# Kernel tuning notes

Measured on AMD Instinct MI355X. Metric: run time of the kernel, lower is better.

## Reference

```python
import jax, jax.numpy as jnp
import numpy as np

B, T, F, H = 256, 1024, 64, 128
DT = 1.0
EPS = 1e-5


def _layer_norm(h, g, b):
    mu = jnp.mean(h, axis=-1, keepdims=True)
    var = jnp.var(h, axis=-1, keepdims=True)
    return (h - mu) * jax.lax.rsqrt(var + EPS) * g + b


def setup_inputs() -> dict:
    key = jax.random.key(0)
    ks = jax.random.split(key, 8)
    def xavier(k, shape):
        fan_in, fan_out = shape[1], shape[0]
        lim = np.sqrt(6.0 / (fan_in + fan_out))
        return jax.random.uniform(k, shape, jnp.float32, -lim, lim)
    return {
        "x": jax.random.normal(ks[0], (B, T, F), jnp.float32),
        # layer 0 (input_dim=F)
        "Wh0": xavier(ks[1], (H, H)), "bh0": jnp.zeros((H,), jnp.float32),
        "Wx0": xavier(ks[2], (H, F)), "bx0": jnp.zeros((H,), jnp.float32),
        "Wt0": xavier(ks[3], (H, F)), "bt0": jnp.zeros((H,), jnp.float32),
        "tau0": jnp.ones((H,), jnp.float32),
        "g0": jnp.ones((H,), jnp.float32), "be0": jnp.zeros((H,), jnp.float32),
        # layer 1 (input_dim=H)
        "Wh1": xavier(ks[4], (H, H)), "bh1": jnp.zeros((H,), jnp.float32),
        "Wx1": xavier(ks[5], (H, H)), "bx1": jnp.zeros((H,), jnp.float32),
        "Wt1": xavier(ks[6], (H, H)), "bt1": jnp.zeros((H,), jnp.float32),
        "tau1": jnp.ones((H,), jnp.float32),
        "g1": jnp.ones((H,), jnp.float32), "be1": jnp.zeros((H,), jnp.float32),
    }


def _cell(x_t, h, Wh, bh, Wx, bx, Wt, bt, tau_base):
    f = jnp.tanh(h @ Wh.T + bh + x_t @ Wx.T + bx)        # (B,H)
    tau = tau_base + jax.nn.softplus(x_t @ Wt.T + bt)     # (B,H)
    return h + (DT / tau) * (-h + f)


def reference(x, Wh0, bh0, Wx0, bx0, Wt0, bt0, tau0, g0, be0,
              Wh1, bh1, Wx1, bx1, Wt1, bt1, tau1, g1, be1):
    xT = jnp.transpose(x, (1, 0, 2))  # (T,B,F)

    def step(carry, x_t):
        h0, h1 = carry
        h0 = _layer_norm(_cell(x_t, h0, Wh0, bh0, Wx0, bx0, Wt0, bt0, tau0), g0, be0)
        h1 = _layer_norm(_cell(h0, h1, Wh1, bh1, Wx1, bx1, Wt1, bt1, tau1), g1, be1)
        return (h0, h1), None

    h_init = (jnp.zeros((x.shape[0], H), x.dtype), jnp.zeros((x.shape[0], H), x.dtype))
    (h0, h1), _ = jax.lax.scan(step, h_init, xT)
    return h1  # hidden_dim == latent_dim, no proj
```

## Files before the change

kernel.cpp:

```cpp
#include <hip/hip_runtime.h>
#include <stdint.h>


#define B_ 256
#define T_ 1024
#define F_ 64
#define H_ 128
#define EPS_ 1e-5f
#define NT_ 512

typedef _Float16 h2 __attribute__((ext_vector_type(2)));
typedef _Float16 h8 __attribute__((ext_vector_type(8)));
typedef float f32x4 __attribute__((ext_vector_type(4)));
typedef __fp16  f16v2 __attribute__((ext_vector_type(2)));

__device__ __forceinline__ h2 pkf16(float a, float b) {
  union { f16v2 f; h2 h; } c;
  c.f = __builtin_amdgcn_cvt_pkrtz(a, b);
  return c.h;
}
__device__ __forceinline__ uint32_t as_u32(h2 h) { union { h2 h; uint32_t u; } c; c.h = h; return c.u; }

__device__ __forceinline__ void wg_barrier() {
  asm volatile("s_waitcnt lgkmcnt(0)\n\ts_barrier" ::: "memory");
}

#if __has_builtin(__builtin_amdgcn_rsqf)
__device__ __forceinline__ float rsq_fast(float x) { return __builtin_amdgcn_rsqf(x); }
#else
__device__ __forceinline__ float rsq_fast(float x) { return rsqrtf(x); }
#endif

#if __has_builtin(__builtin_amdgcn_update_dpp)
template <int CTRL>
__device__ __forceinline__ float dpp_add(float v) {
  union { float f; int i; } a, b;
  a.f = v;
  b.i = __builtin_amdgcn_update_dpp(0, a.i, CTRL, 0xf, 0xf, true);
  return v + b.f;
}
__device__ __forceinline__ float red16(float v) {
  v = dpp_add<0x128>(v);
  v = dpp_add<0x124>(v);
  v = dpp_add<0x122>(v);
  v = dpp_add<0x121>(v);
  return v;
}
#else
__device__ __forceinline__ float red16(float v) {
  v += __shfl_xor(v, 1); v += __shfl_xor(v, 2);
  v += __shfl_xor(v, 4); v += __shfl_xor(v, 8);
  return v;
}
#endif

__device__ __forceinline__ h8 packfrag(const float* p) {
  float4 a = *(const float4*)p;
  float4 b = *(const float4*)(p + 4);
  union { h2 h[4]; h8 v; } c;
  c.h[0] = pkf16(a.x, a.y); c.h[1] = pkf16(a.z, a.w);
  c.h[2] = pkf16(b.x, b.y); c.h[3] = pkf16(b.z, b.w);
  return c.v;
}
__device__ __forceinline__ h8 packfrag_g(const float* w, const float* gv, const float* bv,
                                         float& dg, float& dbe) {
  float4 a = *(const float4*)w;
  float4 b = *(const float4*)(w + 4);
  float4 ga = *(const float4*)gv;
  float4 gb = *(const float4*)(gv + 4);
  float4 ba = *(const float4*)bv;
  float4 bb = *(const float4*)(bv + 4);
  float w0 = a.x*ga.x, w1 = a.y*ga.y, w2 = a.z*ga.z, w3 = a.w*ga.w;
  float w4 = b.x*gb.x, w5 = b.y*gb.y, w6 = b.z*gb.z, w7 = b.w*gb.w;
  dg  += (w0 + w1) + (w2 + w3) + (w4 + w5) + (w6 + w7);
  dbe += a.x*ba.x + a.y*ba.y + a.z*ba.z + a.w*ba.w
       + b.x*bb.x + b.y*bb.y + b.z*bb.z + b.w*bb.w;
  union { h2 h[4]; h8 v; } c;
  c.h[0] = pkf16(w0, w1); c.h[1] = pkf16(w2, w3);
  c.h[2] = pkf16(w4, w5); c.h[3] = pkf16(w6, w7);
  return c.v;
}
__device__ __forceinline__ h8 ldfrag(const uint32_t* p) {
  union { uint4 u; h8 v; } c;
  c.u = *(const uint4*)p;
  return c.v;
}

__device__ __forceinline__ float tanh_fast(float a) {
  float aa = fabsf(a);
  float e  = __expf(2.f * aa);
  float th = 1.f - 2.f * __builtin_amdgcn_rcpf(e + 1.f);
  return copysignf(th, a);
}
__device__ __forceinline__ float softplus_fast(float x) {
  return (x > 20.f) ? x : __logf(1.f + __expf(x));
}

#define MFMA16(A_, B_, C_) __builtin_amdgcn_mfma_f32_16x16x32_f16(A_, B_, C_, 0, 0, 0)

__global__ void __attribute__((amdgpu_flat_work_group_size(NT_, NT_)))
                __attribute__((amdgpu_waves_per_eu(2, 2)))
ltc_scan(
    const float* __restrict__ x,
    const float* __restrict__ Wh0, const float* __restrict__ bh0,
    const float* __restrict__ Wx0, const float* __restrict__ bx0,
    const float* __restrict__ Wt0, const float* __restrict__ bt0,
    const float* __restrict__ tau0, const float* __restrict__ g0,
    const float* __restrict__ be0,
    const float* __restrict__ Wh1, const float* __restrict__ bh1,
    const float* __restrict__ Wx1, const float* __restrict__ bx1,
    const float* __restrict__ Wt1, const float* __restrict__ bt1,
    const float* __restrict__ tau1, const float* __restrict__ g1,
    const float* __restrict__ be1,
    float* __restrict__ out)
{
  __shared__ __align__(16) uint32_t h0p[2][64];
  __shared__ __align__(16) uint32_t h1p[2][64];
  __shared__ __align__(16) uint32_t x4[4][32];
  __shared__ __align__(16) float    part[4][4];

  const int tid = threadIdx.x;
  const int wid = tid >> 6;
  const int l   = tid & 63;
  const int g4  = (l >> 4) << 2;
  const int g8  = (l >> 4) << 3;
  const int b   = blockIdx.x;
  const float* xg = x + (size_t)b * (T_ * F_);
  const bool selT1 = (l & 16) != 0;

  if (tid < 128) { ((uint32_t*)h0p)[tid] = 0u; ((uint32_t*)h1p)[tid] = 0u; }
  if (tid < 16)  ((float*)part)[tid] = 0.f;
  if (tid < 32) {
    float2 a = *(const float2*)(xg + 2 * tid);
    float2 c = *(const float2*)(xg + F_ + 2 * tid);
    x4[0][tid] = as_u32(pkf16(a.x, a.y));
    x4[1][tid] = as_u32(pkf16(c.x, c.y));
  }
  __syncthreads();

  if (wid < 4) {
    const int c0 = wid * 32 + (l & 15);
    const int ct = wid * 32 + (l & 31);
    h8 wh0[4], wh1[4], wx0[2], wx1[2], wt0[2], wt1[2];
    float cg, cb;
    {
      float dg0 = 0.f, db0 = 0.f, dg1 = 0.f, db1 = 0.f;
      const float* p0 = Wh0 + c0 * H_ + g8;
      const float* p1 = Wh0 + (c0 + 16) * H_ + g8;
      #pragma unroll
      for (int m = 0; m < 4; ++m) {
        wh0[m] = packfrag_g(p0 + 32 * m, g0 + g8 + 32 * m, be0 + g8 + 32 * m, dg0, db0);
        wh1[m] = packfrag_g(p1 + 32 * m, g0 + g8 + 32 * m, be0 + g8 + 32 * m, dg1, db1);
      }
      dg0 += __shfl_xor(dg0, 16); dg0 += __shfl_xor(dg0, 32);
      db0 += __shfl_xor(db0, 16); db0 += __shfl_xor(db0, 32);
      dg1 += __shfl_xor(dg1, 16); dg1 += __shfl_xor(dg1, 32);
      db1 += __shfl_xor(db1, 16); db1 += __shfl_xor(db1, 32);
      cg = selT1 ? dg1 : dg0; cb = selT1 ? db1 : db0;
      const float* q0 = Wx0 + c0 * F_ + g8;
      const float* q1 = Wx0 + (c0 + 16) * F_ + g8;
      const float* r0 = Wt0 + c0 * F_ + g8;
      const float* r1 = Wt0 + (c0 + 16) * F_ + g8;
      #pragma unroll
      for (int m = 0; m < 2; ++m) {
        wx0[m] = packfrag(q0 + 32 * m); wx1[m] = packfrag(q1 + 32 * m);
        wt0[m] = packfrag(r0 + 32 * m); wt1[m] = packfrag(r1 + 32 * m);
      }
    }
    const float bhx = bh0[ct] + bx0[ct];
    const float btr = bt0[ct], taub = tau0[ct], gr = g0[ct], ber = be0[ct];
    const int  widx = wid * 16 + ((l & 31) >> 1);
    const bool wlane = ((l & 33) == 0);
    const bool st = (wid == 0) && (l < 32);

    float hcp = 0.f;
    float2 xc0, xc1;
    if (st) {
      xc0 = *(const float2*)(xg + 2 * F_ + 2 * l);
      xc1 = *(const float2*)(xg + 3 * F_ + 2 * l);
    }

    #pragma unroll 4
    for (int i = 0; i <= T_; ++i) {
      const float2 stt = *(const float2*)&part[(i + 3) & 3][0];
      if (st) {
        x4[(i + 2) & 3][l] = as_u32(pkf16(xc0.x, xc0.y));
        xc0 = xc1;
        int tn = (i + 4 < T_) ? (i + 4) : (T_ - 1);
        xc1 = *(const float2*)(xg + tn * F_ + 2 * l);
      }
      const uint32_t* ub = h0p[(i + 1) & 1];
      const uint32_t* xb = x4[i & 3];
      f32x4 aH0 = {0.f,0.f,0.f,0.f}, aH1 = {0.f,0.f,0.f,0.f};
      f32x4 aX0 = {0.f,0.f,0.f,0.f}, aX1 = {0.f,0.f,0.f,0.f};
      f32x4 aT0 = {0.f,0.f,0.f,0.f}, aT1 = {0.f,0.f,0.f,0.f};
      #pragma unroll
      for (int m = 0; m < 4; ++m) {
        h8 af = ldfrag(ub + m * 16 + g4);
        aH0 = MFMA16(af, wh0[m], aH0);
        aH1 = MFMA16(af, wh1[m], aH1);
      }
      #pragma unroll
      for (int m = 0; m < 2; ++m) {
        h8 xf = ldfrag(xb + m * 16 + g4);
        aX0 = MFMA16(xf, wx0[m], aX0);
        aX1 = MFMA16(xf, wx1[m], aX1);
        aT0 = MFMA16(xf, wt0[m], aT0);
        aT1 = MFMA16(xf, wt1[m], aT1);
      }
      float aH = selT1 ? aH1[0] : aH0[0];
      float aX = selT1 ? aX1[0] : aX0[0];
      float aT = selT1 ? aT1[0] : aT0[0];
      float mu = stt.x * (1.f / 128.f);
      float m2 = stt.y * (1.f / 128.f);
      float rstd = rsq_fast(m2 - mu * mu + EPS_);
      float fl = (i > 0) ? 1.f : 0.f;
      float sc = fl * rstd;
      float pa = fmaf(sc, aH, fmaf(-sc * mu, cg, fl * cb)) + aX + bhx;
      float pt = aT + btr;
      float f   = tanh_fast(pa);
      float tau = taub + softplus_fast(pt);
      float hold = fl * fmaf((hcp - mu) * rstd, gr, ber);
      float hc  = fmaf(f - hold, __builtin_amdgcn_rcpf(tau), hold);
      float hc2 = __shfl_xor(hc, 1);
      if (wlane) h0p[i & 1][widx] = as_u32(pkf16(hc, hc2));
      float v = (l & 32) ? hc * hc : hc;
      v = red16(v); v += __shfl_xor(v, 16);
      if (l == 0)  atomicAdd(&part[i & 3][0], v);
      if (l == 32) atomicAdd(&part[i & 3][1], v);
      hcp = hc;
      wg_barrier();
    }
  } else {
    const int c0 = (wid - 4) * 32 + (l & 15);
    const int ct = (wid - 4) * 32 + (l & 31);
    h8 vh0[4], vh1[4], vx0[4], vx1[4], vt0[4], vt1[4];
    float cAg, cAb, cBg, cBb, cTg, cTb;
    {
      float d1=0.f,d2=0.f,d3=0.f,d4=0.f,d5=0.f,d6=0.f;
      float e1=0.f,e2=0.f,e3=0.f,e4=0.f,e5=0.f,e6=0.f;
      const float* p0 = Wh1 + c0 * H_ + g8;
      const float* p1 = Wh1 + (c0 + 16) * H_ + g8;
      const float* q0 = Wx1 + c0 * H_ + g8;
      const float* q1 = Wx1 + (c0 + 16) * H_ + g8;
      const float* r0 = Wt1 + c0 * H_ + g8;
      const float* r1 = Wt1 + (c0 + 16) * H_ + g8;
      #pragma unroll
      for (int m = 0; m < 4; ++m) {
        vh0[m] = packfrag_g(p0 + 32 * m, g1 + g8 + 32 * m, be1 + g8 + 32 * m, d1, d2);
        vh1[m] = packfrag_g(p1 + 32 * m, g1 + g8 + 32 * m, be1 + g8 + 32 * m, e1, e2);
        vx0[m] = packfrag_g(q0 + 32 * m, g0 + g8 + 32 * m, be0 + g8 + 32 * m, d3, d4);
        vx1[m] = packfrag_g(q1 + 32 * m, g0 + g8 + 32 * m, be0 + g8 + 32 * m, e3, e4);
        vt0[m] = packfrag_g(r0 + 32 * m, g0 + g8 + 32 * m, be0 + g8 + 32 * m, d5, d6);
        vt1[m] = packfrag_g(r1 + 32 * m, g0 + g8 + 32 * m, be0 + g8 + 32 * m, e5, e6);
      }
      d1 += __shfl_xor(d1, 16); d1 += __shfl_xor(d1, 32);
      d2 += __shfl_xor(d2, 16); d2 += __shfl_xor(d2, 32);
      d3 += __shfl_xor(d3, 16); d3 += __shfl_xor(d3, 32);
      d4 += __shfl_xor(d4, 16); d4 += __shfl_xor(d4, 32);
      d5 += __shfl_xor(d5, 16); d5 += __shfl_xor(d5, 32);
      d6 += __shfl_xor(d6, 16); d6 += __shfl_xor(d6, 32);
      e1 += __shfl_xor(e1, 16); e1 += __shfl_xor(e1, 32);
      e2 += __shfl_xor(e2, 16); e2 += __shfl_xor(e2, 32);
      e3 += __shfl_xor(e3, 16); e3 += __shfl_xor(e3, 32);
      e4 += __shfl_xor(e4, 16); e4 += __shfl_xor(e4, 32);
      e5 += __shfl_xor(e5, 16); e5 += __shfl_xor(e5, 32);
      e6 += __shfl_xor(e6, 16); e6 += __shfl_xor(e6, 32);
      cAg = selT1 ? e1 : d1; cAb = selT1 ? e2 : d2;
      cBg = selT1 ? e3 : d3; cBb = selT1 ? e4 : d4;
      cTg = selT1 ? e5 : d5; cTb = selT1 ? e6 : d6;
    }
    const float bhx = bh1[ct] + bx1[ct];
    const float btr = bt1[ct], taub = tau1[ct], gr = g1[ct], ber = be1[ct];
    const int  widx = (wid - 4) * 16 + ((l & 31) >> 1);
    const bool wlane = ((l & 33) == 0);
    const bool zt = (tid == NT_ - 1);

    float hcp = 0.f;
    #pragma unroll 2
    for (int i = 0; i <= T_; ++i) {
      const float4 P = *(const float4*)&part[(i + 3) & 3][0];
      if (zt) *(float4*)&part[(i + 2) & 3][0] = make_float4(0.f, 0.f, 0.f, 0.f);
      const uint32_t* u1b = h1p[(i + 1) & 1];
      const uint32_t* u0b = h0p[(i + 1) & 1];
      f32x4 aA0 = {0.f,0.f,0.f,0.f}, aA1 = {0.f,0.f,0.f,0.f};
      f32x4 aB0 = {0.f,0.f,0.f,0.f}, aB1 = {0.f,0.f,0.f,0.f};
      f32x4 aT0 = {0.f,0.f,0.f,0.f}, aT1 = {0.f,0.f,0.f,0.f};
      #pragma unroll
      for (int m = 0; m < 4; ++m) {
        h8 af = ldfrag(u1b + m * 16 + g4);
        aA0 = MFMA16(af, vh0[m], aA0);
        aA1 = MFMA16(af, vh1[m], aA1);
      }
      #pragma unroll
      for (int m = 0; m < 4; ++m) {
        h8 f0 = ldfrag(u0b + m * 16 + g4);
        aB0 = MFMA16(f0, vx0[m], aB0);
        aB1 = MFMA16(f0, vx1[m], aB1);
        aT0 = MFMA16(f0, vt0[m], aT0);
        aT1 = MFMA16(f0, vt1[m], aT1);
      }
      float aA = selT1 ? aA1[0] : aA0[0];
      float aB = selT1 ? aB1[0] : aB0[0];
      float aT = selT1 ? aT1[0] : aT0[0];
      float mu0 = P.x * (1.f / 128.f), m20 = P.y * (1.f / 128.f);
      float mu1 = P.z * (1.f / 128.f), m21 = P.w * (1.f / 128.f);
      float rstd0 = rsq_fast(m20 - mu0 * mu0 + EPS_);
      float rstd1 = rsq_fast(m21 - mu1 * mu1 + EPS_);
      float fl0 = (i > 0) ? 1.f : 0.f;
      float fl1 = (i > 1) ? 1.f : 0.f;
      float sc0 = fl0 * rstd0, sc1 = fl1 * rstd1;
      float pa = fmaf(sc1, aA, fmaf(-sc1 * mu1, cAg, fl1 * cAb))
               + fmaf(sc0, aB, fmaf(-sc0 * mu0, cBg, fl0 * cBb)) + bhx;
      float pt = fmaf(sc0, aT, fmaf(-sc0 * mu0, cTg, fl0 * cTb)) + btr;
      float f   = tanh_fast(pa);
      float tau = taub + softplus_fast(pt);
      float hold = fl1 * fmaf((hcp - mu1) * rstd1, gr, ber);
      float hc  = fmaf(f - hold, __builtin_amdgcn_rcpf(tau), hold);
      float hc2 = __shfl_xor(hc, 1);
      bool we = (i > 0);
      if (we && wlane) h1p[i & 1][widx] = as_u32(pkf16(hc, hc2));
      float v = (l & 32) ? hc * hc : hc;
      v = red16(v); v += __shfl_xor(v, 16);
      if (we && l == 0)  atomicAdd(&part[i & 3][2], v);
      if (we && l == 32) atomicAdd(&part[i & 3][3], v);
      if (we) hcp = hc;
      wg_barrier();
    }
    {
      float mu1 = part[T_ & 3][2] * (1.f / 128.f);
      float m21 = part[T_ & 3][3] * (1.f / 128.f);
      float rstd1 = rsq_fast(m21 - mu1 * mu1 + EPS_);
      float hn = fmaf((hcp - mu1) * rstd1, gr, ber);
      if (l < 32) out[b * H_ + ct] = hn;
    }
  }
}

extern "C" void kernel_launch(void* const* d_in, const int* in_sizes, int n_in,
                              void* d_out, int out_size, void* d_ws, size_t ws_size,
                              hipStream_t stream) {
  const float* x    = (const float*)d_in[0];
  const float* Wh0  = (const float*)d_in[1];
  const float* bh0  = (const float*)d_in[2];
  const float* Wx0  = (const float*)d_in[3];
  const float* bx0  = (const float*)d_in[4];
  const float* Wt0  = (const float*)d_in[5];
  const float* bt0  = (const float*)d_in[6];
  const float* tau0 = (const float*)d_in[7];
  const float* g0   = (const float*)d_in[8];
  const float* be0  = (const float*)d_in[9];
  const float* Wh1  = (const float*)d_in[10];
  const float* bh1  = (const float*)d_in[11];
  const float* Wx1  = (const float*)d_in[12];
  const float* bx1  = (const float*)d_in[13];
  const float* Wt1  = (const float*)d_in[14];
  const float* bt1  = (const float*)d_in[15];
  const float* tau1 = (const float*)d_in[16];
  const float* g1   = (const float*)d_in[17];
  const float* be1  = (const float*)d_in[18];
  float* out        = (float*)d_out;

  ltc_scan<<<B_, NT_, 0, stream>>>(x, Wh0, bh0, Wx0, bx0, Wt0, bt0, tau0, g0, be0,
                                   Wh1, bh1, Wx1, bx1, Wt1, bt1, tau1, g1, be1, out);
}
```

Baseline: 1.009 ms.

## Pass normalized layer-0 state to layer 1 and replace LDS atomics with per-wave partials

Layer-0 waves now write the already layer-normed previous state (hold) into a 4-deep ring buffer, so layer-1 waves can run its input matmul on normalized values and no longer need gamma/beta folding for the Wx/Wt terms or layer-0 statistics. LayerNorm sums are written as per-wave float2 partials and summed by readers, which removes the LDS atomicAdds and the slot-zeroing store. Layer 1 is pipelined one extra step behind, so the loop runs T+2 iterations. The cost is extra LDS traffic, an additional shuffle and store per layer-0 step, and one more barrier iteration.

```diff
diff --git a/kernel.cpp b/kernel.cpp
--- a/kernel.cpp
+++ b/kernel.cpp
@@ -116,8 +116,10 @@
 {
   __shared__ __align__(16) uint32_t h0p[2][64];
   __shared__ __align__(16) uint32_t h1p[2][64];
+  __shared__ __align__(16) uint32_t hn0p[4][64];
   __shared__ __align__(16) uint32_t x4[4][32];
-  __shared__ __align__(16) float    part[4][4];
+  __shared__ __align__(16) float2   p0s[4][4];
+  __shared__ __align__(16) float2   p1s[4][4];
 
   const int tid = threadIdx.x;
   const int wid = tid >> 6;
@@ -129,7 +131,7 @@
   const bool selT1 = (l & 16) != 0;
 
   if (tid < 128) { ((uint32_t*)h0p)[tid] = 0u; ((uint32_t*)h1p)[tid] = 0u; }
-  if (tid < 16)  ((float*)part)[tid] = 0.f;
+  if (tid < 32)  { ((float*)p0s)[tid] = 0.f; ((float*)p1s)[tid] = 0.f; }
   if (tid < 32) {
     float2 a = *(const float2*)(xg + 2 * tid);
     float2 c = *(const float2*)(xg + F_ + 2 * tid);
@@ -181,64 +183,71 @@
     }
 
     #pragma unroll 4
-    for (int i = 0; i <= T_; ++i) {
-      const float2 stt = *(const float2*)&part[(i + 3) & 3][0];
-      if (st) {
-        x4[(i + 2) & 3][l] = as_u32(pkf16(xc0.x, xc0.y));
-        xc0 = xc1;
-        int tn = (i + 4 < T_) ? (i + 4) : (T_ - 1);
-        xc1 = *(const float2*)(xg + tn * F_ + 2 * l);
-      }
-      const uint32_t* ub = h0p[(i + 1) & 1];
-      const uint32_t* xb = x4[i & 3];
-      f32x4 aH0 = {0.f,0.f,0.f,0.f}, aH1 = {0.f,0.f,0.f,0.f};
-      f32x4 aX0 = {0.f,0.f,0.f,0.f}, aX1 = {0.f,0.f,0.f,0.f};
-      f32x4 aT0 = {0.f,0.f,0.f,0.f}, aT1 = {0.f,0.f,0.f,0.f};
-      #pragma unroll
-      for (int m = 0; m < 4; ++m) {
-        h8 af = ldfrag(ub + m * 16 + g4);
-        aH0 = MFMA16(af, wh0[m], aH0);
-        aH1 = MFMA16(af, wh1[m], aH1);
-      }
-      #pragma unroll
-      for (int m = 0; m < 2; ++m) {
-        h8 xf = ldfrag(xb + m * 16 + g4);
-        aX0 = MFMA16(xf, wx0[m], aX0);
-        aX1 = MFMA16(xf, wx1[m], aX1);
-        aT0 = MFMA16(xf, wt0[m], aT0);
-        aT1 = MFMA16(xf, wt1[m], aT1);
-      }
-      float aH = selT1 ? aH1[0] : aH0[0];
-      float aX = selT1 ? aX1[0] : aX0[0];
-      float aT = selT1 ? aT1[0] : aT0[0];
-      float mu = stt.x * (1.f / 128.f);
-      float m2 = stt.y * (1.f / 128.f);
-      float rstd = rsq_fast(m2 - mu * mu + EPS_);
-      float fl = (i > 0) ? 1.f : 0.f;
-      float sc = fl * rstd;
-      float pa = fmaf(sc, aH, fmaf(-sc * mu, cg, fl * cb)) + aX + bhx;
-      float pt = aT + btr;
-      float f   = tanh_fast(pa);
-      float tau = taub + softplus_fast(pt);
-      float hold = fl * fmaf((hcp - mu) * rstd, gr, ber);
-      float hc  = fmaf(f - hold, __builtin_amdgcn_rcpf(tau), hold);
-      float hc2 = __shfl_xor(hc, 1);
-      if (wlane) h0p[i & 1][widx] = as_u32(pkf16(hc, hc2));
-      float v = (l & 32) ? hc * hc : hc;
-      v = red16(v); v += __shfl_xor(v, 16);
-      if (l == 0)  atomicAdd(&part[i & 3][0], v);
-      if (l == 32) atomicAdd(&part[i & 3][1], v);
-      hcp = hc;
+    for (int p = 0; p <= T_ + 1; ++p) {
+      if (p <= T_) {
+        const int i = p;
+        const float4* sp = (const float4*)&p0s[(i + 3) & 3][0];
+        float4 sa = sp[0], sb = sp[1];
+        float ss  = (sa.x + sa.z) + (sb.x + sb.z);
+        float s2s = (sa.y + sa.w) + (sb.y + sb.w);
+        if (st) {
+          x4[(i + 2) & 3][l] = as_u32(pkf16(xc0.x, xc0.y));
+          xc0 = xc1;
+          int tn = (i + 4 < T_) ? (i + 4) : (T_ - 1);
+          xc1 = *(const float2*)(xg + tn * F_ + 2 * l);
+        }
+        const uint32_t* ub = h0p[(i + 1) & 1];
+        const uint32_t* xb = x4[i & 3];
+        f32x4 aH0 = {0.f,0.f,0.f,0.f}, aH1 = {0.f,0.f,0.f,0.f};
+        f32x4 aX0 = {0.f,0.f,0.f,0.f}, aX1 = {0.f,0.f,0.f,0.f};
+        f32x4 aT0 = {0.f,0.f,0.f,0.f}, aT1 = {0.f,0.f,0.f,0.f};
+        #pragma unroll
+        for (int m = 0; m < 4; ++m) {
+          h8 af = ldfrag(ub + m * 16 + g4);
+          aH0 = MFMA16(af, wh0[m], aH0);
+          aH1 = MFMA16(af, wh1[m], aH1);
+        }
+        #pragma unroll
+        for (int m = 0; m < 2; ++m) {
+          h8 xf = ldfrag(xb + m * 16 + g4);
+          aX0 = MFMA16(xf, wx0[m], aX0);
+          aX1 = MFMA16(xf, wx1[m], aX1);
+          aT0 = MFMA16(xf, wt0[m], aT0);
+          aT1 = MFMA16(xf, wt1[m], aT1);
+        }
+        float aH = selT1 ? aH1[0] : aH0[0];
+        float aX = selT1 ? aX1[0] : aX0[0];
+        float aT = selT1 ? aT1[0] : aT0[0];
+        float mu = ss * (1.f / 128.f);
+        float m2 = s2s * (1.f / 128.f);
+        float rstd = rsq_fast(m2 - mu * mu + EPS_);
+        float fl = (i > 0) ? 1.f : 0.f;
+        float sc = fl * rstd;
+        float pa = fmaf(sc, aH, fmaf(-sc * mu, cg, fl * cb)) + aX + bhx;
+        float pt = aT + btr;
+        float f   = tanh_fast(pa);
+        float tau = taub + softplus_fast(pt);
+        float hold = fl * fmaf((hcp - mu) * rstd, gr, ber);
+        float hc  = fmaf(f - hold, __builtin_amdgcn_rcpf(tau), hold);
+        float hn2 = __shfl_xor(hold, 1);
+        if (wlane) hn0p[(i + 3) & 3][widx] = as_u32(pkf16(hold, hn2));
+        float hc2 = __shfl_xor(hc, 1);
+        if (wlane) h0p[i & 1][widx] = as_u32(pkf16(hc, hc2));
+        float v = (l & 32) ? hc * hc : hc;
+        v = red16(v); v += __shfl_xor(v, 16);
+        float v2 = __shfl_down(v, 32);
+        if (l == 0) p0s[i & 3][wid] = make_float2(v, v2);
+        hcp = hc;
+      }
       wg_barrier();
     }
   } else {
     const int c0 = (wid - 4) * 32 + (l & 15);
     const int ct = (wid - 4) * 32 + (l & 31);
     h8 vh0[4], vh1[4], vx0[4], vx1[4], vt0[4], vt1[4];
-    float cAg, cAb, cBg, cBb, cTg, cTb;
+    float cAg, cAb;
     {
-      float d1=0.f,d2=0.f,d3=0.f,d4=0.f,d5=0.f,d6=0.f;
-      float e1=0.f,e2=0.f,e3=0.f,e4=0.f,e5=0.f,e6=0.f;
+      float d1 = 0.f, d2 = 0.f, e1 = 0.f, e2 = 0.f;
       const float* p0 = Wh1 + c0 * H_ + g8;
       const float* p1 = Wh1 + (c0 + 16) * H_ + g8;
       const float* q0 = Wx1 + c0 * H_ + g8;
@@ -249,87 +258,80 @@
       for (int m = 0; m < 4; ++m) {
         vh0[m] = packfrag_g(p0 + 32 * m, g1 + g8 + 32 * m, be1 + g8 + 32 * m, d1, d2);
         vh1[m] = packfrag_g(p1 + 32 * m, g1 + g8 + 32 * m, be1 + g8 + 32 * m, e1, e2);
-        vx0[m] = packfrag_g(q0 + 32 * m, g0 + g8 + 32 * m, be0 + g8 + 32 * m, d3, d4);
-        vx1[m] = packfrag_g(q1 + 32 * m, g0 + g8 + 32 * m, be0 + g8 + 32 * m, e3, e4);
-        vt0[m] = packfrag_g(r0 + 32 * m, g0 + g8 + 32 * m, be0 + g8 + 32 * m, d5, d6);
-        vt1[m] = packfrag_g(r1 + 32 * m, g0 + g8 + 32 * m, be0 + g8 + 32 * m, e5, e6);
+        vx0[m] = packfrag(q0 + 32 * m); vx1[m] = packfrag(q1 + 32 * m);
+        vt0[m] = packfrag(r0 + 32 * m); vt1[m] = packfrag(r1 + 32 * m);
       }
       d1 += __shfl_xor(d1, 16); d1 += __shfl_xor(d1, 32);
       d2 += __shfl_xor(d2, 16); d2 += __shfl_xor(d2, 32);
-      d3 += __shfl_xor(d3, 16); d3 += __shfl_xor(d3, 32);
-      d4 += __shfl_xor(d4, 16); d4 += __shfl_xor(d4, 32);
-      d5 += __shfl_xor(d5, 16); d5 += __shfl_xor(d5, 32);
-      d6 += __shfl_xor(d6, 16); d6 += __shfl_xor(d6, 32);
       e1 += __shfl_xor(e1, 16); e1 += __shfl_xor(e1, 32);
       e2 += __shfl_xor(e2, 16); e2 += __shfl_xor(e2, 32);
-      e3 += __shfl_xor(e3, 16); e3 += __shfl_xor(e3, 32);
-      e4 += __shfl_xor(e4, 16); e4 += __shfl_xor(e4, 32);
-      e5 += __shfl_xor(e5, 16); e5 += __shfl_xor(e5, 32);
-      e6 += __shfl_xor(e6, 16); e6 += __shfl_xor(e6, 32);
       cAg = selT1 ? e1 : d1; cAb = selT1 ? e2 : d2;
-      cBg = selT1 ? e3 : d3; cBb = selT1 ? e4 : d4;
-      cTg = selT1 ? e5 : d5; cTb = selT1 ? e6 : d6;
     }
     const float bhx = bh1[ct] + bx1[ct];
     const float btr = bt1[ct], taub = tau1[ct], gr = g1[ct], ber = be1[ct];
     const int  widx = (wid - 4) * 16 + ((l & 31) >> 1);
     const bool wlane = ((l & 33) == 0);
-    const bool zt = (tid == NT_ - 1);
+    const int  bw = wid - 4;
 
     float hcp = 0.f;
     #pragma unroll 2
-    for (int i = 0; i <= T_; ++i) {
-      const float4 P = *(const float4*)&part[(i + 3) & 3][0];
-      if (zt) *(float4*)&part[(i + 2) & 3][0] = make_float4(0.f, 0.f, 0.f, 0.f);
-      const uint32_t* u1b = h1p[(i + 1) & 1];
-      const uint32_t* u0b = h0p[(i + 1) & 1];
-      f32x4 aA0 = {0.f,0.f,0.f,0.f}, aA1 = {0.f,0.f,0.f,0.f};
-      f32x4 aB0 = {0.f,0.f,0.f,0.f}, aB1 = {0.f,0.f,0.f,0.f};
-      f32x4 aT0 = {0.f,0.f,0.f,0.f}, aT1 = {0.f,0.f,0.f,0.f};
-      #pragma unroll
-      for (int m = 0; m < 4; ++m) {
-        h8 af = ldfrag(u1b + m * 16 + g4);
-        aA0 = MFMA16(af, vh0[m], aA0);
-        aA1 = MFMA16(af, vh1[m], aA1);
-      }
-      #pragma unroll
-      for (int m = 0; m < 4; ++m) {
-        h8 f0 = ldfrag(u0b + m * 16 + g4);
-        aB0 = MFMA16(f0, vx0[m], aB0);
-        aB1 = MFMA16(f0, vx1[m], aB1);
-        aT0 = MFMA16(f0, vt0[m], aT0);
-        aT1 = MFMA16(f0, vt1[m], aT1);
-      }
-      float aA = selT1 ? aA1[0] : aA0[0];
-      float aB = selT1 ? aB1[0] : aB0[0];
-      float aT = selT1 ? aT1[0] : aT0[0];
-      float mu0 = P.x * (1.f / 128.f), m20 = P.y * (1.f / 128.f);
-      float mu1 = P.z * (1.f / 128.f), m21 = P.w * (1.f / 128.f);
-      float rstd0 = rsq_fast(m20 - mu0 * mu0 + EPS_);
-      float rstd1 = rsq_fast(m21 - mu1 * mu1 + EPS_);
-      float fl0 = (i > 0) ? 1.f : 0.f;
-      float fl1 = (i > 1) ? 1.f : 0.f;
-      float sc0 = fl0 * rstd0, sc1 = fl1 * rstd1;
-      float pa = fmaf(sc1, aA, fmaf(-sc1 * mu1, cAg, fl1 * cAb))
-               + fmaf(sc0, aB, fmaf(-sc0 * mu0, cBg, fl0 * cBb)) + bhx;
-      float pt = fmaf(sc0, aT, fmaf(-sc0 * mu0, cTg, fl0 * cTb)) + btr;
-      float f   = tanh_fast(pa);
-      float tau = taub + softplus_fast(pt);
-      float hold = fl1 * fmaf((hcp - mu1) * rstd1, gr, ber);
-      float hc  = fmaf(f - hold, __builtin_amdgcn_rcpf(tau), hold);
-      float hc2 = __shfl_xor(hc, 1);
-      bool we = (i > 0);
-      if (we && wlane) h1p[i & 1][widx] = as_u32(pkf16(hc, hc2));
-      float v = (l & 32) ? hc * hc : hc;
-      v = red16(v); v += __shfl_xor(v, 16);
-      if (we && l == 0)  atomicAdd(&part[i & 3][2], v);
-      if (we && l == 32) atomicAdd(&part[i & 3][3], v);
-      if (we) hcp = hc;
+    for (int p = 0; p <= T_ + 1; ++p) {
+      if (p >= 2) {
+        const int j = p - 2;
+        const float4* sp = (const float4*)&p1s[(j + 3) & 3][0];
+        float4 sa = sp[0], sb = sp[1];
+        float ss1 = (sa.x + sa.z) + (sb.x + sb.z);
+        float s21 = (sa.y + sa.w) + (sb.y + sb.w);
+        const uint32_t* u1b = h1p[(j + 1) & 1];
+        const uint32_t* hnb = hn0p[j & 3];
+        f32x4 aA0 = {0.f,0.f,0.f,0.f}, aA1 = {0.f,0.f,0.f,0.f};
+        f32x4 aB0 = {0.f,0.f,0.f,0.f}, aB1 = {0.f,0.f,0.f,0.f};
+        f32x4 aT0 = {0.f,0.f,0.f,0.f}, aT1 = {0.f,0.f,0.f,0.f};
+        #pragma unroll
+        for (int m = 0; m < 4; ++m) {
+          h8 af = ldfrag(u1b + m * 16 + g4);
+          aA0 = MFMA16(af, vh0[m], aA0);
+          aA1 = MFMA16(af, vh1[m], aA1);
+        }
+        #pragma unroll
+        for (int m = 0; m < 4; ++m) {
+          h8 f0 = ldfrag(hnb + m * 16 + g4);
+          aB0 = MFMA16(f0, vx0[m], aB0);
+          aB1 = MFMA16(f0, vx1[m], aB1);
+          aT0 = MFMA16(f0, vt0[m], aT0);
+          aT1 = MFMA16(f0, vt1[m], aT1);
+        }
+        float aA = selT1 ? aA1[0] : aA0[0];
+        float aB = selT1 ? aB1[0] : aB0[0];
+        float aT = selT1 ? aT1[0] : aT0[0];
+        float mu1 = ss1 * (1.f / 128.f);
+        float m21 = s21 * (1.f / 128.f);
+        float rstd1 = rsq_fast(m21 - mu1 * mu1 + EPS_);
+        float fl1 = (j > 0) ? 1.f : 0.f;
+        float sc1 = fl1 * rstd1;
+        float pa = fmaf(sc1, aA, fmaf(-sc1 * mu1, cAg, fl1 * cAb)) + aB + bhx;
+        float pt = aT + btr;
+        float f   = tanh_fast(pa);
+        float tau = taub + softplus_fast(pt);
+        float hold = fl1 * fmaf((hcp - mu1) * rstd1, gr, ber);
+        float hc  = fmaf(f - hold, __builtin_amdgcn_rcpf(tau), hold);
+        float hc2 = __shfl_xor(hc, 1);
+        if (wlane) h1p[j & 1][widx] = as_u32(pkf16(hc, hc2));
+        float v = (l & 32) ? hc * hc : hc;
+        v = red16(v); v += __shfl_xor(v, 16);
+        float v2 = __shfl_down(v, 32);
+        if (l == 0) p1s[j & 3][bw] = make_float2(v, v2);
+        hcp = hc;
+      }
       wg_barrier();
     }
     {
-      float mu1 = part[T_ & 3][2] * (1.f / 128.f);
-      float m21 = part[T_ & 3][3] * (1.f / 128.f);
+      const float4* sp = (const float4*)&p1s[(T_ - 1) & 3][0];
+      float4 sa = sp[0], sb = sp[1];
+      float ss1 = (sa.x + sa.z) + (sb.x + sb.z);
+      float s21 = (sa.y + sa.w) + (sb.y + sb.w);
+      float mu1 = ss1 * (1.f / 128.f);
+      float m21 = s21 * (1.f / 128.f);
       float rstd1 = rsq_fast(m21 - mu1 * mu1 + EPS_);
       float hn = fmaf((hcp - mu1) * rstd1, gr, ber);
       if (l < 32) out[b * H_ + ct] = hn;
```

Result: faster. 875.8 us (-13.2%).
